# Performance work log

Measured on AMD Instinct MI355X. Metric: run time of the kernel, lower is better.

The kernel has to match this reference:

```python
import jax, jax.numpy as jnp
import numpy as np

N_NODES = 50000
N_EDGES = 800000
IN_CH = 128
HID = 64
OUT_CH = 10
N_GRAPHS = 512


def setup_inputs() -> dict:
    key = jax.random.key(0)
    ks = jax.random.split(key, 16)
    x = jax.random.normal(ks[0], (N_NODES, IN_CH), dtype=jnp.float32)
    edge_index = jax.random.randint(ks[1], (2, N_EDGES), 0, N_NODES, dtype=jnp.int64)
    batch = jnp.sort(jax.random.randint(ks[2], (N_NODES,), 0, N_GRAPHS, dtype=jnp.int64))
    def lin(k, fan_in, fan_out):
        bound = 1.0 / np.sqrt(fan_in)
        kw, kb = jax.random.split(k)
        w = jax.random.uniform(kw, (fan_in, fan_out), minval=-bound, maxval=bound, dtype=jnp.float32)
        b = jax.random.uniform(kb, (fan_out,), minval=-bound, maxval=bound, dtype=jnp.float32)
        return w, b
    w0a, b0a = lin(ks[3], IN_CH, HID)
    w0b, b0b = lin(ks[4], HID, HID)
    w1a, b1a = lin(ks[5], HID, HID)
    w1b, b1b = lin(ks[6], HID, HID)
    fcw, fcb = lin(ks[7], HID, OUT_CH)
    eps0 = jnp.zeros((), dtype=jnp.float32)  # train_eps=True, init 0
    eps1 = jnp.zeros((), dtype=jnp.float32)
    return {"x": x, "edge_index": edge_index, "batch": batch,
            "eps0": eps0, "w0a": w0a, "b0a": b0a, "w0b": w0b, "b0b": b0b,
            "eps1": eps1, "w1a": w1a, "b1a": b1a, "w1b": w1b, "b1b": b1b,
            "fcw": fcw, "fcb": fcb}


def _gin_layer(x, src, dst, eps, wa, ba, wb, bb):
    # sum-aggregate neighbor messages: agg[i] = sum_{(j->i) in E} x[j]
    agg = jax.ops.segment_sum(x[src], dst, num_segments=N_NODES)
    h = (1.0 + eps) * x + agg
    h = jax.nn.relu(h @ wa + ba)
    h = jax.nn.relu(h @ wb + bb)  # MLP ends in ReLU; outer F.relu is a no-op
    return h


def reference(x, edge_index, batch, eps0, w0a, b0a, w0b, b0b,
              eps1, w1a, b1a, w1b, b1b, fcw, fcb):
    src, dst = edge_index[0], edge_index[1]
    h = _gin_layer(x, src, dst, eps0, w0a, b0a, w0b, b0b)
    # dropout skipped (inference)
    h = _gin_layer(h, src, dst, eps1, w1a, b1a, w1b, b1b)
    pooled = jax.ops.segment_sum(h, batch, num_segments=N_GRAPHS)  # [G, HID]
    logits = pooled @ fcw + fcb
    return jax.nn.log_softmax(logits, axis=1)
```

## Files before the change

kernel.cpp:

```cpp
#include <hip/hip_runtime.h>
#include <math.h>

#define IN_CH 128
#define HID 64
#define OUT_CH 10
#define LINB 1051
#define W_LIN 5
#define W_CNT 2

typedef unsigned int uint32;
typedef unsigned char u8;
typedef unsigned short bf16u;
typedef __attribute__((ext_vector_type(8))) short bf16x8;
typedef __attribute__((ext_vector_type(4))) float f32x4;
typedef __attribute__((ext_vector_type(2))) float f32x2;

static __device__ inline bf16u f2bf(float f) {
    uint32 u = __float_as_uint(f);
    u += 0x7fff + ((u >> 16) & 1);
    return (bf16u)(u >> 16);
}
static __device__ inline uint32 pack2(float a, float b) {
    return (uint32)f2bf(a) | ((uint32)f2bf(b) << 16);
}
static __device__ inline u8 f2fp8(float v) {
    uint32 p = __builtin_amdgcn_cvt_pk_fp8_f32(v, v, 0, false);
    return (u8)(p & 0xff);
}
static __device__ inline void acc_fp8x4(uint32 u, float& a0, float& a1,
                                        float& a2, float& a3) {
    f32x2 lo = __builtin_amdgcn_cvt_pk_f32_fp8((int)u, false);
    f32x2 hi = __builtin_amdgcn_cvt_pk_f32_fp8((int)u, true);
    a0 += lo.x; a1 += lo.y; a2 += hi.x; a3 += hi.y;
}

static __device__ inline void gather_group(
    const uint32* __restrict__ y8, const int* __restrict__ col,
    int rs, int re, int c2,
    float& a0, float& a1, float& a2, float& a3)
{
    int j = rs;
    for (; j + 4 <= re; j += 4) {
        int s0 = col[j];
        int s1 = col[j + 1];
        int s2 = col[j + 2];
        int s3 = col[j + 3];
        uint32 u0 = y8[s0 * 16 + c2];
        uint32 u1 = y8[s1 * 16 + c2];
        uint32 u2 = y8[s2 * 16 + c2];
        uint32 u3 = y8[s3 * 16 + c2];
        acc_fp8x4(u0, a0, a1, a2, a3);
        acc_fp8x4(u1, a0, a1, a2, a3);
        acc_fp8x4(u2, a0, a1, a2, a3);
        acc_fp8x4(u3, a0, a1, a2, a3);
    }
    for (; j < re; ++j) {
        uint32 u = y8[col[j] * 16 + c2];
        acc_fp8x4(u, a0, a1, a2, a3);
    }
}

__global__ __launch_bounds__(256, 6) void k_pre(
    const int* __restrict__ dst, int* __restrict__ cnt, int* __restrict__ pos,
    const float4* __restrict__ x4, const float* __restrict__ w,
    u8* __restrict__ y, int N, int E, int nb)
{
    int tid = threadIdx.x;
    int bid = blockIdx.x;
    if (bid >= LINB) {
        int ncb = nb - LINB;
        for (int e = (bid - LINB) * 256 + tid; e < E; e += ncb * 256)
            pos[e] = atomicAdd(&cnt[dst[e]], 1);
    }

    __shared__ __align__(16) uint32 t32[16 * 68];
    int wid = tid >> 6, lane = tid & 63;
    int quad = lane >> 4, n15 = lane & 15;
    int mycol = wid * 16 + n15;
    bf16x8 fb[4];
    #pragma unroll
    for (int s = 0; s < 4; s++)
        #pragma unroll
        for (int j = 0; j < 8; j++)
            fb[s][j] = (short)f2bf(w[(s * 32 + quad * 8 + j) * HID + mycol]);
    int snode = tid >> 4, sk = tid & 15;

    int NG = (N + 15) >> 4;
    long TW   = (long)LINB * W_LIN + (long)(nb - LINB) * W_CNT;
    long cum0 = (bid <= LINB) ? (long)bid * W_LIN
                              : (long)LINB * W_LIN + (long)(bid - LINB) * W_CNT;
    long cum1 = cum0 + ((bid < LINB) ? W_LIN : W_CNT);
    int gs = (int)(cum0 * NG / TW);
    int ge = (int)(cum1 * NG / TW);

    for (int g = gs; g < ge; ++g) {
        long g0 = (long)g * 16;
        long node = g0 + snode;
        if (node < N) {
            float4 v0 = x4[node * 32 + sk * 2];
            float4 v1 = x4[node * 32 + sk * 2 + 1];
            uint32 p[4] = {pack2(v0.x, v0.y), pack2(v0.z, v0.w),
                           pack2(v1.x, v1.y), pack2(v1.z, v1.w)};
            *(uint4*)((char*)t32 + snode * 272 + sk * 16) = *(uint4*)p;
        }
        __syncthreads();
        f32x4 acc = {0.f, 0.f, 0.f, 0.f};
        #pragma unroll
        for (int s = 0; s < 4; s++) {
            bf16x8 a = *(const bf16x8*)((const char*)t32 + n15 * 272 + s * 64 + quad * 16);
            acc = __builtin_amdgcn_mfma_f32_16x16x32_bf16(a, fb[s], acc, 0, 0, 0);
        }
        #pragma unroll
        for (int r = 0; r < 4; r++) {
            long n = g0 + quad * 4 + r;
            if (n < N) y[n * HID + mycol] = f2fp8(acc[r]);
        }
        __syncthreads();
    }
}

__global__ __launch_bounds__(256) void k_scan(
    const int* __restrict__ cnt, int* __restrict__ row_ptr,
    int* __restrict__ partials, int* __restrict__ counter, int N, int E, int nch)
{
    __shared__ int red[256];
    int tid = threadIdx.x;
    int bid = blockIdx.x;
    long base = (long)bid * 1024 + tid * 4;
    int v[4]; int s = 0;
    #pragma unroll
    for (int i = 0; i < 4; i++) {
        long idx = base + i;
        v[i] = (idx < N) ? cnt[idx] : 0;
        s += v[i];
    }
    red[tid] = s;
    __syncthreads();
    for (int off = 1; off < 256; off <<= 1) {
        int t = (tid >= off) ? red[tid - off] : 0;
        __syncthreads();
        red[tid] += t;
        __syncthreads();
    }
    int myexcl = red[tid] - s;
    if (tid == 255) {
        __hip_atomic_store(&partials[bid], red[255], __ATOMIC_RELEASE,
                           __HIP_MEMORY_SCOPE_AGENT);
        atomicAdd(counter, 1);
    }
    if (tid == 0) {
        while (__hip_atomic_load(counter, __ATOMIC_ACQUIRE,
                                 __HIP_MEMORY_SCOPE_AGENT) < nch) { }
    }
    __syncthreads();
    int off = 0;
    for (int i = tid; i < bid; i += 256)
        off += __hip_atomic_load(&partials[i], __ATOMIC_RELAXED,
                                 __HIP_MEMORY_SCOPE_AGENT);
    __syncthreads();
    red[tid] = off;
    __syncthreads();
    for (int o = 128; o; o >>= 1) {
        if (tid < o) red[tid] += red[tid + o];
        __syncthreads();
    }
    int run = red[0] + myexcl;
    #pragma unroll
    for (int i = 0; i < 4; i++) {
        long idx = base + i;
        if (idx < N) row_ptr[idx] = run;
        run += v[i];
    }
    if (bid == 0 && tid == 0) row_ptr[N] = E;
}

__global__ __launch_bounds__(256) void k_place(
    const int* __restrict__ src, const int* __restrict__ dst,
    const int* __restrict__ row_ptr, const int* __restrict__ pos,
    int* __restrict__ col, int E)
{
    int e = blockIdx.x * 256 + threadIdx.x;
    if (e >= E) return;
    col[row_ptr[dst[e]] + pos[e]] = src[e];
}

__global__ __launch_bounds__(256, 6) void k_agg0f(
    const uint32* __restrict__ y8, const int* __restrict__ row_ptr,
    const int* __restrict__ col, const float* __restrict__ epsp,
    const float* __restrict__ ba, const float* __restrict__ wb,
    const float* __restrict__ bb, const float* __restrict__ w1a,
    u8* __restrict__ y1, int N)
{
    __shared__ __align__(16) uint32 t32[16 * 36];
    __shared__ __align__(16) uint32 h32[16 * 36];
    int tid = threadIdx.x;
    int wid = tid >> 6, lane = tid & 63;
    int c2 = lane & 15, h = lane >> 4;
    int quad = lane >> 4, n15 = lane & 15;
    int n0 = wid * 4;
    int mycol = wid * 16 + n15;
    float e = 1.f + epsp[0];
    float4 bav = ((const float4*)ba)[c2];
    float bbv = bb[mycol];
    bf16x8 fb[2], f1[2];
    #pragma unroll
    for (int s = 0; s < 2; s++)
        #pragma unroll
        for (int j = 0; j < 8; j++) {
            fb[s][j] = (short)f2bf(wb[(s * 32 + quad * 8 + j) * HID + mycol]);
            f1[s][j] = (short)f2bf(w1a[(s * 32 + quad * 8 + j) * HID + mycol]);
        }
    for (long g0 = (long)blockIdx.x * 16; g0 < N; g0 += (long)gridDim.x * 16) {
        long node = g0 + n0 + h;
        if (node < N) {
            int rs = row_ptr[node], re = row_ptr[node + 1];
            uint32 us = y8[node * 16 + c2];
            float a0 = 0.f, a1 = 0.f, a2 = 0.f, a3 = 0.f;
            gather_group(y8, col, rs, re, c2, a0, a1, a2, a3);
            f32x2 lo = __builtin_amdgcn_cvt_pk_f32_fp8((int)us, false);
            f32x2 hi = __builtin_amdgcn_cvt_pk_f32_fp8((int)us, true);
            a0 = fmaf(e, lo.x, a0); a1 = fmaf(e, lo.y, a1);
            a2 = fmaf(e, hi.x, a2); a3 = fmaf(e, hi.y, a3);
            t32[(n0 + h) * 36 + 2 * c2]     = pack2(fmaxf(a0 + bav.x, 0.f),
                                                    fmaxf(a1 + bav.y, 0.f));
            t32[(n0 + h) * 36 + 2 * c2 + 1] = pack2(fmaxf(a2 + bav.z, 0.f),
                                                    fmaxf(a3 + bav.w, 0.f));
        }
        __syncthreads();
        f32x4 acc = {bbv, bbv, bbv, bbv};
        {
            bf16x8 a0 = *(const bf16x8*)((const char*)t32 + n15 * 144 + quad * 16);
            bf16x8 a1 = *(const bf16x8*)((const char*)t32 + n15 * 144 + 64 + quad * 16);
            acc = __builtin_amdgcn_mfma_f32_16x16x32_bf16(a0, fb[0], acc, 0, 0, 0);
            acc = __builtin_amdgcn_mfma_f32_16x16x32_bf16(a1, fb[1], acc, 0, 0, 0);
        }
        #pragma unroll
        for (int r = 0; r < 4; r++)
            ((short*)h32)[(quad * 4 + r) * 72 + mycol] = (short)f2bf(fmaxf(acc[r], 0.f));
        __syncthreads();
        f32x4 acc2 = {0.f, 0.f, 0.f, 0.f};
        {
            bf16x8 a0 = *(const bf16x8*)((const char*)h32 + n15 * 144 + quad * 16);
            bf16x8 a1 = *(const bf16x8*)((const char*)h32 + n15 * 144 + 64 + quad * 16);
            acc2 = __builtin_amdgcn_mfma_f32_16x16x32_bf16(a0, f1[0], acc2, 0, 0, 0);
            acc2 = __builtin_amdgcn_mfma_f32_16x16x32_bf16(a1, f1[1], acc2, 0, 0, 0);
        }
        #pragma unroll
        for (int r = 0; r < 4; r++) {
            long n = g0 + quad * 4 + r;
            if (n < N) y1[n * HID + mycol] = f2fp8(acc2[r]);
        }
    }
}

__global__ __launch_bounds__(256, 6) void k_agg1(
    const uint32* __restrict__ y8, const int* __restrict__ row_ptr,
    const int* __restrict__ col, const float* __restrict__ epsp,
    const float* __restrict__ ba, const float* __restrict__ wb,
    const float* __restrict__ bb, const int* __restrict__ batch,
    float* __restrict__ pooled, int N)
{
    __shared__ __align__(16) uint32 t32[16 * 36];
    int tid = threadIdx.x;
    int wid = tid >> 6, lane = tid & 63;
    int c2 = lane & 15, h = lane >> 4;
    int quad = lane >> 4, n15 = lane & 15;
    int n0 = wid * 4;
    int mycol = wid * 16 + n15;
    float e = 1.f + epsp[0];
    float4 bav = ((const float4*)ba)[c2];
    float bbv = bb[mycol];
    bf16x8 fb[2];
    #pragma unroll
    for (int s = 0; s < 2; s++)
        #pragma unroll
        for (int j = 0; j < 8; j++)
            fb[s][j] = (short)f2bf(wb[(s * 32 + quad * 8 + j) * HID + mycol]);
    for (long g0 = (long)blockIdx.x * 16; g0 < N; g0 += (long)gridDim.x * 16) {
        long node = g0 + n0 + h;
        if (node < N) {
            int rs = row_ptr[node], re = row_ptr[node + 1];
            uint32 us = y8[node * 16 + c2];
            float a0 = 0.f, a1 = 0.f, a2 = 0.f, a3 = 0.f;
            gather_group(y8, col, rs, re, c2, a0, a1, a2, a3);
            f32x2 lo = __builtin_amdgcn_cvt_pk_f32_fp8((int)us, false);
            f32x2 hi = __builtin_amdgcn_cvt_pk_f32_fp8((int)us, true);
            a0 = fmaf(e, lo.x, a0); a1 = fmaf(e, lo.y, a1);
            a2 = fmaf(e, hi.x, a2); a3 = fmaf(e, hi.y, a3);
            t32[(n0 + h) * 36 + 2 * c2]     = pack2(fmaxf(a0 + bav.x, 0.f),
                                                    fmaxf(a1 + bav.y, 0.f));
            t32[(n0 + h) * 36 + 2 * c2 + 1] = pack2(fmaxf(a2 + bav.z, 0.f),
                                                    fmaxf(a3 + bav.w, 0.f));
        }
        __syncthreads();
        f32x4 acc = {bbv, bbv, bbv, bbv};
        {
            bf16x8 a0 = *(const bf16x8*)((const char*)t32 + n15 * 144 + quad * 16);
            bf16x8 a1 = *(const bf16x8*)((const char*)t32 + n15 * 144 + 64 + quad * 16);
            acc = __builtin_amdgcn_mfma_f32_16x16x32_bf16(a0, fb[0], acc, 0, 0, 0);
            acc = __builtin_amdgcn_mfma_f32_16x16x32_bf16(a1, fb[1], acc, 0, 0, 0);
        }
        float rv[4];
        #pragma unroll
        for (int r = 0; r < 4; r++) rv[r] = fmaxf(acc[r], 0.f);
        int nv = (int)((N - g0) < 16 ? (N - g0) : 16);
        int bf_ = batch[g0], bl_ = batch[g0 + nv - 1];
        if (bf_ == bl_) {
            float s = 0.f;
            #pragma unroll
            for (int r = 0; r < 4; r++)
                if (quad * 4 + r < nv) s += rv[r];
            s += __shfl_xor(s, 16);
            s += __shfl_xor(s, 32);
            if (quad == 0)
                atomicAdd(&pooled[(long)bf_ * HID + mycol], s);
        } else {
            #pragma unroll
            for (int r = 0; r < 4; r++) {
                long n = g0 + quad * 4 + r;
                if (n < N)
                    atomicAdd(&pooled[(long)batch[n] * HID + mycol], rv[r]);
            }
        }
        __syncthreads();
    }
}

__global__ __launch_bounds__(64) void k_head(
    const float* __restrict__ pooled, const float* __restrict__ fcw,
    const float* __restrict__ fcb, float* __restrict__ out)
{
    int g = blockIdx.x;
    int l = threadIdx.x;
    float logit = -INFINITY;
    if (l < OUT_CH) {
        float acc = fcb[l];
        #pragma unroll
        for (int k = 0; k < HID; k++)
            acc = fmaf(pooled[g * HID + k], fcw[k * OUT_CH + l], acc);
        logit = acc;
    }
    float m = logit;
    #pragma unroll
    for (int off = 32; off; off >>= 1) m = fmaxf(m, __shfl_xor(m, off));
    float ex = (l < OUT_CH) ? expf(logit - m) : 0.0f;
    float s = ex;
    #pragma unroll
    for (int off = 32; off; off >>= 1) s += __shfl_xor(s, off);
    if (l < OUT_CH) out[g * OUT_CH + l] = logit - m - logf(s);
}

extern "C" void kernel_launch(void* const* d_in, const int* in_sizes, int n_in,
                              void* d_out, int out_size, void* d_ws, size_t ws_size,
                              hipStream_t stream) {
    const float* x    = (const float*)d_in[0];
    const int*   ei   = (const int*)d_in[1];
    const int*   batch= (const int*)d_in[2];
    const float* eps0 = (const float*)d_in[3];
    const float* w0a  = (const float*)d_in[4];
    const float* b0a  = (const float*)d_in[5];
    const float* w0b  = (const float*)d_in[6];
    const float* b0b  = (const float*)d_in[7];
    const float* eps1 = (const float*)d_in[8];
    const float* w1a  = (const float*)d_in[9];
    const float* b1a  = (const float*)d_in[10];
    const float* w1b  = (const float*)d_in[11];
    const float* b1b  = (const float*)d_in[12];
    const float* fcw  = (const float*)d_in[13];
    const float* fcb  = (const float*)d_in[14];
    float* out = (float*)d_out;

    const int N = in_sizes[0] / IN_CH;
    const int E = in_sizes[1] / 2;
    const int G = out_size / OUT_CH;
    const int* src = ei;
    const int* dst = ei + E;

    char* ws = (char*)d_ws;
    int*    row_ptr  = (int*)(ws);
    int*    colv     = (int*)(ws + 200064);
    u8*     y0       = (u8*)(ws + 3400064);
    u8*     y1       = (u8*)(ws + 6600064);
    int*    cnt      = (int*)(ws + 9800064);
    int*    counter  = (int*)(ws + 10000064);
    int*    partials = (int*)(ws + 10000128);
    float*  pooled   = (float*)(ws + 10000384);
    int*    pos      = (int*)(ws + 10131456);

    hipMemsetAsync(cnt, 0, 331392, stream);

    int eb = (E + 255) / 256;
    int nb = (N + 31) / 32;
    int nch = (N + 1023) / 1024;
    k_pre<<<nb, 256, 0, stream>>>(dst, cnt, pos, (const float4*)x, w0a, y0,
                                  N, E, nb);
    k_scan<<<nch, 256, 0, stream>>>(cnt, row_ptr, partials, counter, N, E, nch);
    k_place<<<eb, 256, 0, stream>>>(src, dst, row_ptr, pos, colv, E);

    k_agg0f<<<nb, 256, 0, stream>>>((const uint32*)y0, row_ptr, colv, eps0,
                                    b0a, w0b, b0b, w1a, y1, N);
    k_agg1<<<nb, 256, 0, stream>>>((const uint32*)y1, row_ptr, colv, eps1,
                                   b1a, w1b, b1b, batch, pooled, N);
    k_head<<<G, 64, 0, stream>>>(pooled, fcw, fcb, out);
}
```

Baseline: 195.8 us.

## Split first linear layer across pre and place kernels to overlap CSR build

The layer-0 linear projection (x @ w0a to fp8) was done entirely in k_pre alongside the degree counting. It is now split in half: k_pre computes the first half of node groups, and the CSR placement kernel is merged with the second half so scatter blocks and GEMM blocks run concurrently. This aims to balance work between the atomic counting, the placement scatter and the dense projection, hiding memory-bound scatter behind compute. The risk is that k_place now runs with fewer blocks in a grid-stride loop, and the work split weights may be off.

```diff
diff --git a/kernel.cpp b/kernel.cpp
--- a/kernel.cpp
+++ b/kernel.cpp
@@ -60,6 +60,50 @@
     }
 }
 
+static __device__ inline void lin0_group(
+    const float4* __restrict__ x4, const bf16x8* fb, u8* __restrict__ y,
+    uint32* t32, int tid, long g0, int N)
+{
+    int wid = tid >> 6, lane = tid & 63;
+    int quad = lane >> 4, n15 = lane & 15;
+    int mycol = wid * 16 + n15;
+    int snode = tid >> 4, sk = tid & 15;
+    long node = g0 + snode;
+    if (node < N) {
+        float4 v0 = x4[node * 32 + sk * 2];
+        float4 v1 = x4[node * 32 + sk * 2 + 1];
+        uint32 p[4] = {pack2(v0.x, v0.y), pack2(v0.z, v0.w),
+                       pack2(v1.x, v1.y), pack2(v1.z, v1.w)};
+        *(uint4*)((char*)t32 + snode * 272 + sk * 16) = *(uint4*)p;
+    }
+    __syncthreads();
+    f32x4 acc = {0.f, 0.f, 0.f, 0.f};
+    #pragma unroll
+    for (int s = 0; s < 4; s++) {
+        bf16x8 a = *(const bf16x8*)((const char*)t32 + n15 * 272 + s * 64 + quad * 16);
+        acc = __builtin_amdgcn_mfma_f32_16x16x32_bf16(a, fb[s], acc, 0, 0, 0);
+    }
+    #pragma unroll
+    for (int r = 0; r < 4; r++) {
+        long n = g0 + quad * 4 + r;
+        if (n < N) y[n * HID + mycol] = f2fp8(acc[r]);
+    }
+    __syncthreads();
+}
+
+static __device__ inline void load_w0(const float* __restrict__ w, bf16x8* fb,
+                                      int tid)
+{
+    int wid = tid >> 6, lane = tid & 63;
+    int quad = lane >> 4, n15 = lane & 15;
+    int mycol = wid * 16 + n15;
+    #pragma unroll
+    for (int s = 0; s < 4; s++)
+        #pragma unroll
+        for (int j = 0; j < 8; j++)
+            fb[s][j] = (short)f2bf(w[(s * 32 + quad * 8 + j) * HID + mycol]);
+}
+
 __global__ __launch_bounds__(256, 6) void k_pre(
     const int* __restrict__ dst, int* __restrict__ cnt, int* __restrict__ pos,
     const float4* __restrict__ x4, const float* __restrict__ w,
@@ -74,49 +118,19 @@
     }
 
     __shared__ __align__(16) uint32 t32[16 * 68];
-    int wid = tid >> 6, lane = tid & 63;
-    int quad = lane >> 4, n15 = lane & 15;
-    int mycol = wid * 16 + n15;
     bf16x8 fb[4];
-    #pragma unroll
-    for (int s = 0; s < 4; s++)
-        #pragma unroll
-        for (int j = 0; j < 8; j++)
-            fb[s][j] = (short)f2bf(w[(s * 32 + quad * 8 + j) * HID + mycol]);
-    int snode = tid >> 4, sk = tid & 15;
-
-    int NG = (N + 15) >> 4;
+    load_w0(w, fb, tid);
+
+    int NG  = (N + 15) >> 4;
+    int NGH = (NG + 1) >> 1;
     long TW   = (long)LINB * W_LIN + (long)(nb - LINB) * W_CNT;
     long cum0 = (bid <= LINB) ? (long)bid * W_LIN
                               : (long)LINB * W_LIN + (long)(bid - LINB) * W_CNT;
     long cum1 = cum0 + ((bid < LINB) ? W_LIN : W_CNT);
-    int gs = (int)(cum0 * NG / TW);
-    int ge = (int)(cum1 * NG / TW);
-
-    for (int g = gs; g < ge; ++g) {
-        long g0 = (long)g * 16;
-        long node = g0 + snode;
-        if (node < N) {
-            float4 v0 = x4[node * 32 + sk * 2];
-            float4 v1 = x4[node * 32 + sk * 2 + 1];
-            uint32 p[4] = {pack2(v0.x, v0.y), pack2(v0.z, v0.w),
-                           pack2(v1.x, v1.y), pack2(v1.z, v1.w)};
-            *(uint4*)((char*)t32 + snode * 272 + sk * 16) = *(uint4*)p;
-        }
-        __syncthreads();
-        f32x4 acc = {0.f, 0.f, 0.f, 0.f};
-        #pragma unroll
-        for (int s = 0; s < 4; s++) {
-            bf16x8 a = *(const bf16x8*)((const char*)t32 + n15 * 272 + s * 64 + quad * 16);
-            acc = __builtin_amdgcn_mfma_f32_16x16x32_bf16(a, fb[s], acc, 0, 0, 0);
-        }
-        #pragma unroll
-        for (int r = 0; r < 4; r++) {
-            long n = g0 + quad * 4 + r;
-            if (n < N) y[n * HID + mycol] = f2fp8(acc[r]);
-        }
-        __syncthreads();
-    }
+    int gs = (int)(cum0 * NGH / TW);
+    int ge = (int)(cum1 * NGH / TW);
+    for (int g = gs; g < ge; ++g)
+        lin0_group(x4, fb, y, t32, tid, (long)g * 16, N);
 }
 
 __global__ __launch_bounds__(256) void k_scan(
@@ -174,14 +188,33 @@
     if (bid == 0 && tid == 0) row_ptr[N] = E;
 }
 
-__global__ __launch_bounds__(256) void k_place(
+__global__ __launch_bounds__(256, 6) void k_placelin0(
     const int* __restrict__ src, const int* __restrict__ dst,
     const int* __restrict__ row_ptr, const int* __restrict__ pos,
-    int* __restrict__ col, int E)
-{
-    int e = blockIdx.x * 256 + threadIdx.x;
-    if (e >= E) return;
-    col[row_ptr[dst[e]] + pos[e]] = src[e];
+    int* __restrict__ col,
+    const float4* __restrict__ x4, const float* __restrict__ w,
+    u8* __restrict__ y, int N, int E, int nb)
+{
+    int tid = threadIdx.x;
+    int bid = blockIdx.x;
+    if (bid >= LINB) {
+        int ncb = nb - LINB;
+        for (int e = (bid - LINB) * 256 + tid; e < E; e += ncb * 256)
+            col[row_ptr[dst[e]] + pos[e]] = src[e];
+        return;
+    }
+
+    __shared__ __align__(16) uint32 t32[16 * 68];
+    bf16x8 fb[4];
+    load_w0(w, fb, tid);
+
+    int NG  = (N + 15) >> 4;
+    int NGH = (NG + 1) >> 1;
+    int rem = NG - NGH;
+    int gs = NGH + (int)((long)bid * rem / LINB);
+    int ge = NGH + (int)((long)(bid + 1) * rem / LINB);
+    for (int g = gs; g < ge; ++g)
+        lin0_group(x4, fb, y, t32, tid, (long)g * 16, N);
 }
 
 __global__ __launch_bounds__(256, 6) void k_agg0f(
@@ -389,14 +422,13 @@
 
     hipMemsetAsync(cnt, 0, 331392, stream);
 
-    int eb = (E + 255) / 256;
     int nb = (N + 31) / 32;
     int nch = (N + 1023) / 1024;
     k_pre<<<nb, 256, 0, stream>>>(dst, cnt, pos, (const float4*)x, w0a, y0,
                                   N, E, nb);
     k_scan<<<nch, 256, 0, stream>>>(cnt, row_ptr, partials, counter, N, E, nch);
-    k_place<<<eb, 256, 0, stream>>>(src, dst, row_ptr, pos, colv, E);
-
+    k_placelin0<<<nb, 256, 0, stream>>>(src, dst, row_ptr, pos, colv,
+                                        (const float4*)x, w0a, y0, N, E, nb);
     k_agg0f<<<nb, 256, 0, stream>>>((const uint32*)y0, row_ptr, colv, eps0,
                                     b0a, w0b, b0b, w1a, y1, N);
     k_agg1<<<nb, 256, 0, stream>>>((const uint32*)y1, row_ptr, colv, eps1,
```

Result: no change. 197.1 us (+0.6%).
